# Optimization experiments

Hardware: AMD Instinct MI355X
Metric: run time of the kernel (lower is better)

Reference implementation:

```python
import jax, jax.numpy as jnp
import numpy as np

B, T, D = 4, 2048, 1024
H = 16            # N_HEADS
HD = D // H       # head_dim = 64
VD = 64           # VALUE_DIM


def setup_inputs() -> dict:
    key = jax.random.key(0)
    ks = jax.random.split(key, 9)
    s_in = 1.0 / np.sqrt(D)
    s_out = 1.0 / np.sqrt(H * VD)
    x = jax.random.normal(ks[0], (B, T, D), dtype=jnp.float32)
    # stacked per-head projection weights (nn.Linear applies x @ W.T; we store [in,out])
    Wq = jax.random.uniform(ks[1], (H, D, HD), jnp.float32, -s_in, s_in)
    bq = jax.random.uniform(ks[2], (H, HD), jnp.float32, -s_in, s_in)
    Wk = jax.random.uniform(ks[3], (H, D, HD), jnp.float32, -s_in, s_in)
    bk = jax.random.uniform(ks[4], (H, HD), jnp.float32, -s_in, s_in)
    Wv = jax.random.uniform(ks[5], (H, D, VD), jnp.float32, -s_in, s_in)
    bv = jax.random.uniform(ks[6], (H, VD), jnp.float32, -s_in, s_in)
    Wo = jax.random.uniform(ks[7], (H * VD, D), jnp.float32, -s_out, s_out)
    bo = jax.random.uniform(ks[8], (D,), jnp.float32, -s_out, s_out)
    return {"x": x, "Wq": Wq, "bq": bq, "Wk": Wk, "bk": bk,
            "Wv": Wv, "bv": bv, "Wo": Wo, "bo": bo}


def reference(x, Wq, bq, Wk, bk, Wv, bv, Wo, bo):
    b, t, d = x.shape
    scale = HD ** -0.5
    # per-head projections, vectorized over heads
    q = jnp.einsum('btd,hdk->bhtk', x, Wq) + bq[None, :, None, :]
    k = jnp.einsum('btd,hdk->bhtk', x, Wk) + bk[None, :, None, :]
    v = jnp.einsum('btd,hdv->bhtv', x, Wv) + bv[None, :, None, :]
    scores = jnp.einsum('bhsk,bhtk->bhst', q, k) * scale
    causal = jnp.triu(jnp.ones((t, t), dtype=bool), k=1)  # mask[i,j]=j>i
    scores = jnp.where(causal, -jnp.inf, scores)
    attn = jax.nn.softmax(scores, axis=-1)  # dropout = identity in eval
    out = jnp.einsum('bhst,bhtv->bhsv', attn, v)
    concat = out.transpose(0, 2, 1, 3).reshape(b, t, H * VD)  # cat over heads
    return concat @ Wo + bo
```

## Files before the change

### kernel.cpp

```cpp
#include <hip/hip_runtime.h>

#define Bc 4
#define Tc 2048
#define Dc 1024
#define Hc 16
#define HDc 64
#define VDc 64
#define MTOT (Bc * Tc)
#define NQKV 3072

typedef __attribute__((ext_vector_type(8))) short short8;
typedef __attribute__((ext_vector_type(4))) short short4_;
typedef __attribute__((ext_vector_type(4))) float float4_;

#define QSCALE 0.18033688011112042f

static __device__ __forceinline__ short f2bf(float f) {
  unsigned u = __builtin_bit_cast(unsigned, f);
  u += 0x7fffu + ((u >> 16) & 1u);
  return (short)(u >> 16);
}

static __device__ __forceinline__ void gload16(const void* g, void* l) {
  __builtin_amdgcn_global_load_lds(
      (__attribute__((address_space(1))) void*)(unsigned long long)g,
      (__attribute__((address_space(3))) void*)l, 16, 0, 0);
}


__global__ void cvt_x_kernel(const float* __restrict__ x, short* __restrict__ xb) {
  int i = blockIdx.x * blockDim.x + threadIdx.x;
  float4_ v = reinterpret_cast<const float4_*>(x)[i];
  short4_ o;
  o[0] = f2bf(v[0]); o[1] = f2bf(v[1]); o[2] = f2bf(v[2]); o[3] = f2bf(v[3]);
  reinterpret_cast<short4_*>(xb)[i] = o;
}

__global__ __launch_bounds__(256) void build_wqkv_kernel(
    const float* __restrict__ Wq, const float* __restrict__ Wk,
    const float* __restrict__ Wv, const float* __restrict__ bq,
    const float* __restrict__ bk, const float* __restrict__ bv,
    short* __restrict__ wt, float* __restrict__ bias) {
  __shared__ __align__(16) short Lt[64][72];
  const int tid = threadIdx.x;
  const int mat = blockIdx.x >> 4, h = blockIdx.x & 15;
  const float* W  = (mat == 0) ? Wq : (mat == 1) ? Wk : Wv;
  const float* bs = (mat == 0) ? bq : (mat == 1) ? bk : bv;
  const int base_n = (mat << 10) + (h << 6);
  if (blockIdx.y == 0 && tid < 64) bias[base_n + tid] = bs[h * 64 + tid];
  for (int dc = 0; dc < 4; dc++) {
    const int d0 = blockIdx.y * 256 + dc * 64;
#pragma unroll
    for (int rep = 0; rep < 16; rep++) {
      int dl = rep * 4 + (tid >> 6);
      int hd = tid & 63;
      Lt[hd][dl] = f2bf(W[(size_t)(h * 1024 + d0 + dl) * 64 + hd]);
    }
    __syncthreads();
    int hd = tid >> 2, c = tid & 3;
    short8 v0 = *(const short8*)&Lt[hd][c * 16];
    short8 v1 = *(const short8*)&Lt[hd][c * 16 + 8];
    *(short8*)&wt[(size_t)(base_n + hd) * 1024 + d0 + c * 16] = v0;
    *(short8*)&wt[(size_t)(base_n + hd) * 1024 + d0 + c * 16 + 8] = v1;
    __syncthreads();
  }
}

__global__ __launch_bounds__(256) void build_wo_kernel(
    const float* __restrict__ Wo, short* __restrict__ wot) {
  __shared__ __align__(16) short Lt[64][72];
  const int tid = threadIdx.x;
  const int n0 = blockIdx.x * 64, k0 = blockIdx.y * 64;
#pragma unroll
  for (int rep = 0; rep < 16; rep++) {
    int kl = rep * 4 + (tid >> 6);
    int nl = tid & 63;
    Lt[nl][kl] = f2bf(Wo[(size_t)(k0 + kl) * 1024 + n0 + nl]);
  }
  __syncthreads();
  int nl = tid >> 2, c = tid & 3;
  short8 v0 = *(const short8*)&Lt[nl][c * 16];
  short8 v1 = *(const short8*)&Lt[nl][c * 16 + 8];
  *(short8*)&wot[(size_t)(n0 + nl) * 1024 + k0 + c * 16] = v0;
  *(short8*)&wot[(size_t)(n0 + nl) * 1024 + k0 + c * 16 + 8] = v1;
}

#define GEMM_PREAMBLE                                                          \
  __shared__ __align__(16) short As[128 * 32];                                 \
  __shared__ __align__(16) short Bs[128 * 32];                                 \
  const int tid = threadIdx.x;                                                 \
  const int wave = tid >> 6, lane = tid & 63;                                  \
  const int lm = lane & 15, quad = lane >> 4;                                  \
  const int wm = (wave & 1) * 64, wn = (wave >> 1) * 64;                       \
  const int srow = tid >> 2, pchunk = tid & 3;                                 \
  const int swr = (srow ^ (srow >> 2)) & 3;                                    \
  const int pq = quad ^ ((lm ^ (lm >> 2)) & 3);                                \
  const short* Ag = A + (size_t)(m0 + srow) * 1024 + (pchunk ^ swr) * 8;       \
  const short* Bg = Bt + (size_t)(n0 + srow) * 1024 + (pchunk ^ swr) * 8;      \
  short* Al = As + wave * 512;                                                 \
  short* Bl = Bs + wave * 512;                                                 \
  float4_ acc[4][4] = {};                                                      \
  for (int k0 = 0; k0 < 1024; k0 += 32) {                                      \
    gload16(Ag + k0, Al);                                                      \
    gload16(Ag + 64 * 1024 + k0, Al + 2048);                                   \
    gload16(Bg + k0, Bl);                                                      \
    gload16(Bg + 64 * 1024 + k0, Bl + 2048);                                   \
    __syncthreads();                                                           \
    short8 af[4], bf[4];                                                       \
    _Pragma("unroll") for (int i = 0; i < 4; i++) {                            \
      af[i] = *(const short8*)&As[(wm + i * 16 + lm) * 32 + pq * 8];           \
      bf[i] = *(const short8*)&Bs[(wn + i * 16 + lm) * 32 + pq * 8];           \
    }                                                                          \
    _Pragma("unroll") for (int i = 0; i < 4; i++)                              \
      _Pragma("unroll") for (int j = 0; j < 4; j++)                            \
        acc[i][j] = __builtin_amdgcn_mfma_f32_16x16x32_bf16(af[i], bf[j],      \
                                                            acc[i][j], 0, 0, 0); \
    __syncthreads();                                                           \
  }

__global__ __launch_bounds__(256) void gemm_qkv_kernel(
    const short* __restrict__ A, const short* __restrict__ Bt,
    const float* __restrict__ bias,
    short* __restrict__ Qb, short* __restrict__ Kb, short* __restrict__ Vt) {
  const int m0 = blockIdx.x * 128, n0 = blockIdx.y * 128;
  GEMM_PREAMBLE
#pragma unroll
  for (int j = 0; j < 4; j++) {
    int n = n0 + wn + j * 16 + lm;
    int mat = n >> 10, h = (n >> 6) & 15, hd = n & 63;
    float bv = bias[n];
    float sc = (mat == 0) ? QSCALE : 1.0f;
#pragma unroll
    for (int i = 0; i < 4; i++) {
#pragma unroll
      for (int r = 0; r < 4; r++) {
        int m = m0 + wm + i * 16 + quad * 4 + r;
        int b = m >> 11, t = m & (Tc - 1);
        int bh = b * Hc + h;
        short val = f2bf((acc[i][j][r] + bv) * sc);
        if (mat == 0)      Qb[((size_t)bh * Tc + t) * HDc + hd] = val;
        else if (mat == 1) Kb[((size_t)bh * Tc + t) * HDc + hd] = val;
        else               Vt[((size_t)bh * VDc + hd) * Tc + t] = val;
      }
    }
  }
}

__global__ __launch_bounds__(256) void gemm_out_kernel(
    const short* __restrict__ A, const short* __restrict__ Bt,
    const float* __restrict__ bo, float* __restrict__ out) {
  const int m0 = blockIdx.x * 128, n0 = blockIdx.y * 128;
  GEMM_PREAMBLE
#pragma unroll
  for (int j = 0; j < 4; j++) {
    int n = n0 + wn + j * 16 + lm;
    float bv = bo[n];
#pragma unroll
    for (int i = 0; i < 4; i++) {
#pragma unroll
      for (int r = 0; r < 4; r++) {
        int m = m0 + wm + i * 16 + quad * 4 + r;
        out[(size_t)m * Dc + n] = acc[i][j][r] + bv;
      }
    }
  }
}

__global__ __launch_bounds__(512) void attn_kernel(
    const short* __restrict__ Qb, const short* __restrict__ Kb,
    const short* __restrict__ Vt, short* __restrict__ AO) {
  __shared__ __align__(16) short Ks[2][64 * 64];
  __shared__ __align__(16) short Vs[2][64 * 64];
  __shared__ __align__(16) short Pbuf[8][32 * 64];
  const int tid = threadIdx.x;
  const int wave = tid >> 6, lane = tid & 63;
  const int lm = lane & 15, quad = lane >> 4;
  const int bh = blockIdx.y;
  const int qblk = (blockIdx.y < 32) ? (7 - blockIdx.x) : blockIdx.x;
  const int q0 = qblk * 256 + wave * 32;

  const short* Qp = Qb + (size_t)bh * Tc * HDc;
  const short* Kp = Kb + (size_t)bh * Tc * HDc;
  const short* Vp = Vt + (size_t)bh * VDc * Tc;
  short* pb = Pbuf[wave];

  const int srow = tid >> 3;
  const int chlog = (tid & 7) ^ (srow & 7);
  const int sw = lm & 7;

  short8 qf[2][2];
#pragma unroll
  for (int g = 0; g < 2; g++)
#pragma unroll
    for (int h = 0; h < 2; h++)
      qf[g][h] = *reinterpret_cast<const short8*>(Qp + (q0 + g * 16 + lm) * HDc + h * 32 + quad * 8);

  float4_ o[4][2] = {};
  float lsum[2] = {0.f, 0.f};

  const int nt = 4 * qblk + 4;
  gload16(Kp + (size_t)srow * HDc + chlog * 8, &Ks[0][wave * 512]);
  gload16(Vp + (size_t)srow * Tc + chlog * 8, &Vs[0][wave * 512]);

  for (int it = 0; it < nt; ++it) {
    const int kt = it << 6;
    const int cur = it & 1;
    __syncthreads();
    if (it + 1 < nt) {
      const int ktn = kt + 64;
      gload16(Kp + (size_t)(ktn + srow) * HDc + chlog * 8, &Ks[1 - cur][wave * 512]);
      gload16(Vp + (size_t)srow * Tc + ktn + chlog * 8, &Vs[1 - cur][wave * 512]);
    }
    if (kt > q0 + 31) continue;
    const short* Kt = Ks[cur];
    const short* Vtl = Vs[cur];

    float4_ st[4][2] = {};
#pragma unroll
    for (int mf = 0; mf < 4; ++mf) {
      int row = mf * 16 + lm;
      short8 k0 = *(const short8*)&Kt[row * 64 + (quad ^ sw) * 8];
      short8 k1 = *(const short8*)&Kt[row * 64 + ((4 + quad) ^ sw) * 8];
#pragma unroll
      for (int g = 0; g < 2; ++g) {
        st[mf][g] = __builtin_amdgcn_mfma_f32_16x16x32_bf16(k0, qf[g][0], st[mf][g], 0, 0, 0);
        st[mf][g] = __builtin_amdgcn_mfma_f32_16x16x32_bf16(k1, qf[g][1], st[mf][g], 0, 0, 0);
      }
    }

    if (kt + 63 > q0) {
#pragma unroll
      for (int mf = 0; mf < 4; ++mf)
#pragma unroll
        for (int g = 0; g < 2; ++g) {
          int qrow = q0 + g * 16 + lm;
#pragma unroll
          for (int r = 0; r < 4; ++r) {
            int key = kt + mf * 16 + quad * 4 + r;
            if (key > qrow) st[mf][g][r] = -1e30f;
          }
        }
    }

#pragma unroll
    for (int g = 0; g < 2; ++g) {
      float sum = 0.f;
#pragma unroll
      for (int mf = 0; mf < 4; ++mf) {
        float p0 = __builtin_amdgcn_exp2f(st[mf][g][0]);
        float p1 = __builtin_amdgcn_exp2f(st[mf][g][1]);
        float p2 = __builtin_amdgcn_exp2f(st[mf][g][2]);
        float p3 = __builtin_amdgcn_exp2f(st[mf][g][3]);
        sum += (p0 + p1) + (p2 + p3);
        short4_ pk;
        pk[0] = f2bf(p0); pk[1] = f2bf(p1); pk[2] = f2bf(p2); pk[3] = f2bf(p3);
        *(short4_*)&pb[(g * 16 + lm) * 64 + ((mf * 2 + (quad >> 1)) ^ sw) * 8 + (quad & 1) * 4] = pk;
      }
      lsum[g] += sum;
    }
    __asm__ volatile("s_waitcnt lgkmcnt(0)" ::: "memory");

    short8 pf[2][2];
#pragma unroll
    for (int g = 0; g < 2; ++g)
#pragma unroll
      for (int h = 0; h < 2; ++h)
        pf[g][h] = *reinterpret_cast<const short8*>(&pb[(g * 16 + lm) * 64 + ((h * 4 + quad) ^ sw) * 8]);

#pragma unroll
    for (int mf2 = 0; mf2 < 4; ++mf2) {
      int row = mf2 * 16 + lm;
      short8 v0 = *(const short8*)&Vtl[row * 64 + (quad ^ sw) * 8];
      short8 v1 = *(const short8*)&Vtl[row * 64 + ((4 + quad) ^ sw) * 8];
#pragma unroll
      for (int g = 0; g < 2; ++g) {
        o[mf2][g] = __builtin_amdgcn_mfma_f32_16x16x32_bf16(v0, pf[g][0], o[mf2][g], 0, 0, 0);
        o[mf2][g] = __builtin_amdgcn_mfma_f32_16x16x32_bf16(v1, pf[g][1], o[mf2][g], 0, 0, 0);
      }
    }
  }

#pragma unroll
  for (int g = 0; g < 2; ++g) {
    lsum[g] += __shfl_xor(lsum[g], 16);
    lsum[g] += __shfl_xor(lsum[g], 32);
  }

  const int b = bh >> 4, h = bh & 15;
  float inv0 = 1.0f / lsum[0], inv1 = 1.0f / lsum[1];
#pragma unroll
  for (int g = 0; g < 2; ++g) {
    float inv = g ? inv1 : inv0;
#pragma unroll
    for (int mf2 = 0; mf2 < 4; ++mf2) {
      short4_ pk;
      pk[0] = f2bf(o[mf2][g][0] * inv); pk[1] = f2bf(o[mf2][g][1] * inv);
      pk[2] = f2bf(o[mf2][g][2] * inv); pk[3] = f2bf(o[mf2][g][3] * inv);
      *(short4_*)&pb[(g * 16 + lm) * 64 + ((mf2 * 2 + (quad >> 1)) ^ sw) * 8 + (quad & 1) * 4] = pk;
    }
  }
  __asm__ volatile("s_waitcnt lgkmcnt(0)" ::: "memory");
#pragma unroll
  for (int p = 0; p < 4; ++p) {
    int lr = p * 8 + (lane >> 3);
    short8 vv = *reinterpret_cast<const short8*>(&pb[lr * 64 + (((lane & 7) ^ (lr & 7))) * 8]);
    *reinterpret_cast<short8*>(AO + ((size_t)(b * Tc + q0 + lr)) * 1024 + h * 64 + (lane & 7) * 8) = vv;
  }
}

extern "C" void kernel_launch(void* const* d_in, const int* in_sizes, int n_in,
                              void* d_out, int out_size, void* d_ws, size_t ws_size,
                              hipStream_t stream) {
  const float* x  = (const float*)d_in[0];
  const float* Wq = (const float*)d_in[1];
  const float* bq = (const float*)d_in[2];
  const float* Wk = (const float*)d_in[3];
  const float* bk = (const float*)d_in[4];
  const float* Wv = (const float*)d_in[5];
  const float* bv = (const float*)d_in[6];
  const float* Wo = (const float*)d_in[7];
  const float* bo = (const float*)d_in[8];
  float* out = (float*)d_out;

  char* ws = (char*)d_ws;
  size_t off = 0;
  short* xb   = (short*)(ws + off); off += (size_t)MTOT * Dc * 2;
  short* wqkv = (short*)(ws + off); off += (size_t)NQKV * Dc * 2;
  float* bqkv = (float*)(ws + off); off += ((size_t)NQKV * 4 + 255) & ~255ull;
  short* Qb   = (short*)(ws + off); off += (size_t)Bc * Hc * Tc * HDc * 2;
  short* Kb   = (short*)(ws + off); off += (size_t)Bc * Hc * Tc * HDc * 2;
  short* Vt   = (short*)(ws + off); off += (size_t)Bc * Hc * VDc * Tc * 2;
  short* AO   = (short*)(ws + off); off += (size_t)MTOT * 1024 * 2;
  short* wot  = (short*)(ws + off); off += (size_t)Dc * Dc * 2;

  cvt_x_kernel<<<MTOT * Dc / (256 * 4), 256, 0, stream>>>(x, xb);
  build_wqkv_kernel<<<dim3(48, 4), 256, 0, stream>>>(Wq, Wk, Wv, bq, bk, bv, wqkv, bqkv);
  build_wo_kernel<<<dim3(16, 16), 256, 0, stream>>>(Wo, wot);
  gemm_qkv_kernel<<<dim3(MTOT / 128, NQKV / 128), 256, 0, stream>>>(xb, wqkv, bqkv, Qb, Kb, Vt);
  attn_kernel<<<dim3(8, Bc * Hc), 512, 0, stream>>>(Qb, Kb, Vt, AO);
  gemm_out_kernel<<<dim3(MTOT / 128, Dc / 128), 256, 0, stream>>>(AO, wot, bo, out);
}
```

Baseline: 276.0 us.

## Double-buffer GEMM LDS tiles and stage QKV epilogue through shared memory

The GEMM K-loop now uses two LDS buffers, prefetching the next K-slice while the current one is consumed, which removes one barrier per iteration and overlaps global loads with MFMA work. The QKV epilogue writes each wave's tile into LDS and then emits 16-byte coalesced stores for Q/K rows and transposed V rows, replacing scattered 2-byte stores. This raises LDS use per block (about 36 KB for QKV), which may lower occupancy.

```diff
diff --git a/kernel.cpp b/kernel.cpp
--- a/kernel.cpp
+++ b/kernel.cpp
@@ -85,9 +85,8 @@
   *(short8*)&wot[(size_t)(n0 + nl) * 1024 + k0 + c * 16 + 8] = v1;
 }
 
-#define GEMM_PREAMBLE                                                          \
-  __shared__ __align__(16) short As[128 * 32];                                 \
-  __shared__ __align__(16) short Bs[128 * 32];                                 \
+#define GEMM_KLOOP(SHSZ)                                                       \
+  __shared__ __align__(16) short Sh[SHSZ];                                     \
   const int tid = threadIdx.x;                                                 \
   const int wave = tid >> 6, lane = tid & 63;                                  \
   const int lm = lane & 15, quad = lane >> 4;                                  \
@@ -97,25 +96,32 @@
   const int pq = quad ^ ((lm ^ (lm >> 2)) & 3);                                \
   const short* Ag = A + (size_t)(m0 + srow) * 1024 + (pchunk ^ swr) * 8;       \
   const short* Bg = Bt + (size_t)(n0 + srow) * 1024 + (pchunk ^ swr) * 8;      \
-  short* Al = As + wave * 512;                                                 \
-  short* Bl = Bs + wave * 512;                                                 \
   float4_ acc[4][4] = {};                                                      \
+  gload16(Ag, &Sh[wave * 512]);                                                \
+  gload16(Ag + 64 * 1024, &Sh[2048 + wave * 512]);                             \
+  gload16(Bg, &Sh[4096 + wave * 512]);                                         \
+  gload16(Bg + 64 * 1024, &Sh[6144 + wave * 512]);                             \
   for (int k0 = 0; k0 < 1024; k0 += 32) {                                      \
-    gload16(Ag + k0, Al);                                                      \
-    gload16(Ag + 64 * 1024 + k0, Al + 2048);                                   \
-    gload16(Bg + k0, Bl);                                                      \
-    gload16(Bg + 64 * 1024 + k0, Bl + 2048);                                   \
+    const int cb = (k0 >> 5) & 1;                                              \
     __syncthreads();                                                           \
+    if (k0 + 32 < 1024) {                                                      \
+      short* d = &Sh[(1 - cb) * 8192];                                         \
+      gload16(Ag + k0 + 32, d + wave * 512);                                   \
+      gload16(Ag + 64 * 1024 + k0 + 32, d + 2048 + wave * 512);                \
+      gload16(Bg + k0 + 32, d + 4096 + wave * 512);                            \
+      gload16(Bg + 64 * 1024 + k0 + 32, d + 6144 + wave * 512);                \
+    }                                                                          \
+    const short* Ab = &Sh[cb * 8192];                                          \
+    const short* Bb = &Sh[cb * 8192 + 4096];                                   \
     short8 af[4], bf[4];                                                       \
     _Pragma("unroll") for (int i = 0; i < 4; i++) {                            \
-      af[i] = *(const short8*)&As[(wm + i * 16 + lm) * 32 + pq * 8];           \
-      bf[i] = *(const short8*)&Bs[(wn + i * 16 + lm) * 32 + pq * 8];           \
+      af[i] = *(const short8*)&Ab[(wm + i * 16 + lm) * 32 + pq * 8];           \
+      bf[i] = *(const short8*)&Bb[(wn + i * 16 + lm) * 32 + pq * 8];           \
     }                                                                          \
     _Pragma("unroll") for (int i = 0; i < 4; i++)                              \
       _Pragma("unroll") for (int j = 0; j < 4; j++)                            \
         acc[i][j] = __builtin_amdgcn_mfma_f32_16x16x32_bf16(af[i], bf[j],      \
                                                             acc[i][j], 0, 0, 0); \
-    __syncthreads();                                                           \
   }
 
 __global__ __launch_bounds__(256) void gemm_qkv_kernel(
@@ -123,25 +129,51 @@
     const float* __restrict__ bias,
     short* __restrict__ Qb, short* __restrict__ Kb, short* __restrict__ Vt) {
   const int m0 = blockIdx.x * 128, n0 = blockIdx.y * 128;
-  GEMM_PREAMBLE
-#pragma unroll
-  for (int j = 0; j < 4; j++) {
-    int n = n0 + wn + j * 16 + lm;
-    int mat = n >> 10, h = (n >> 6) & 15, hd = n & 63;
-    float bv = bias[n];
-    float sc = (mat == 0) ? QSCALE : 1.0f;
-#pragma unroll
-    for (int i = 0; i < 4; i++) {
-#pragma unroll
-      for (int r = 0; r < 4; r++) {
-        int m = m0 + wm + i * 16 + quad * 4 + r;
-        int b = m >> 11, t = m & (Tc - 1);
-        int bh = b * Hc + h;
-        short val = f2bf((acc[i][j][r] + bv) * sc);
-        if (mat == 0)      Qb[((size_t)bh * Tc + t) * HDc + hd] = val;
-        else if (mat == 1) Kb[((size_t)bh * Tc + t) * HDc + hd] = val;
-        else               Vt[((size_t)bh * VDc + hd) * Tc + t] = val;
-      }
+  GEMM_KLOOP(18432)
+  __syncthreads();
+  short* epi = &Sh[wave * 4608];
+  const int mat = n0 >> 10;
+  const int hh = ((n0 + wn) >> 6) & 15;
+  const int b = m0 >> 11;
+  const int bh = b * Hc + hh;
+  const int t0 = (m0 & (Tc - 1)) + wm;
+  if (mat < 2) {
+    const float sc = (mat == 0) ? QSCALE : 1.0f;
+#pragma unroll
+    for (int j = 0; j < 4; j++) {
+      float bvs = bias[n0 + wn + j * 16 + lm] * sc;
+#pragma unroll
+      for (int i = 0; i < 4; i++)
+#pragma unroll
+        for (int r = 0; r < 4; r++)
+          epi[(i * 16 + quad * 4 + r) * 72 + j * 16 + lm] = f2bf(acc[i][j][r] * sc + bvs);
+    }
+    __asm__ volatile("s_waitcnt lgkmcnt(0)" ::: "memory");
+    short* dst = (mat == 0) ? Qb : Kb;
+#pragma unroll
+    for (int p = 0; p < 8; p++) {
+      int lrow = p * 8 + (lane >> 3);
+      short8 v = *(const short8*)&epi[lrow * 72 + (lane & 7) * 8];
+      *(short8*)&dst[((size_t)bh * Tc + t0 + lrow) * HDc + (lane & 7) * 8] = v;
+    }
+  } else {
+#pragma unroll
+    for (int j = 0; j < 4; j++) {
+      float bv = bias[n0 + wn + j * 16 + lm];
+#pragma unroll
+      for (int i = 0; i < 4; i++) {
+        short4_ pk;
+#pragma unroll
+        for (int r = 0; r < 4; r++) pk[r] = f2bf(acc[i][j][r] + bv);
+        *(short4_*)&epi[(j * 16 + lm) * 72 + i * 16 + quad * 4] = pk;
+      }
+    }
+    __asm__ volatile("s_waitcnt lgkmcnt(0)" ::: "memory");
+#pragma unroll
+    for (int p = 0; p < 8; p++) {
+      int hdrow = p * 8 + (lane >> 3);
+      short8 v = *(const short8*)&epi[hdrow * 72 + (lane & 7) * 8];
+      *(short8*)&Vt[((size_t)bh * VDc + hdrow) * Tc + t0 + (lane & 7) * 8] = v;
     }
   }
 }
@@ -150,7 +182,7 @@
     const short* __restrict__ A, const short* __restrict__ Bt,
     const float* __restrict__ bo, float* __restrict__ out) {
   const int m0 = blockIdx.x * 128, n0 = blockIdx.y * 128;
-  GEMM_PREAMBLE
+  GEMM_KLOOP(16384)
 #pragma unroll
   for (int j = 0; j < 4; j++) {
     int n = n0 + wn + j * 16 + lm;
```

Result: faster. 256.9 us (-6.9%).
